# Performance work log

Measured on AMD Instinct MI355X. Metric: run time of the kernel, lower is better.

Reference implementation:

```python
import jax, jax.numpy as jnp
import numpy as np

N = 50000      # nodes
E = 800000     # edges (before self-loops)
B = 512        # graphs in batch
IN, HID, OUT, HEADS = 768, 256, 128, 4
NEG_SLOPE = 0.2
EPS = 1e-16


def glorot(key, shape):
    fan = shape[0] + shape[-1]
    return jax.random.normal(key, shape, jnp.float32) * jnp.sqrt(2.0 / fan)


def setup_inputs() -> dict:
    key = jax.random.key(0)
    ks = jax.random.split(key, 12)
    d1, d2 = HID // HEADS, OUT // HEADS
    return {
        "x": jax.random.normal(ks[0], (N, IN), jnp.float32),
        "edge_index": jax.random.randint(ks[1], (2, E), 0, N),
        "batch": jnp.sort(jax.random.randint(ks[2], (N,), 0, B)),
        # conv1: GATConv(IN, HID//HEADS, heads=HEADS)
        "W1": glorot(ks[3], (IN, HID)),
        "att_src1": glorot(ks[4], (HEADS, d1)),
        "att_dst1": glorot(ks[5], (HEADS, d1)),
        "b1": jnp.zeros((HID,), jnp.float32),
        # conv2: GATConv(HID+IN, OUT//HEADS, heads=HEADS)
        "W2": glorot(ks[6], (HID + IN, OUT)),
        "att_src2": glorot(ks[7], (HEADS, d2)),
        "att_dst2": glorot(ks[8], (HEADS, d2)),
        "b2": jnp.zeros((OUT,), jnp.float32),
    }


def gat_conv(x, src, dst, W, att_src, att_dst, bias):
    # PyG GATConv (concat heads): h = x @ W, e_ij = LeakyReLU(a_s.h_j + a_d.h_i),
    # alpha = softmax over incoming edges of each destination node.
    n = x.shape[0]
    heads, d = att_src.shape
    h = (x @ W).reshape(n, heads, d)                          # [N,H,D]
    a_s = jnp.einsum('nhd,hd->nh', h, att_src)                # [N,H]
    a_d = jnp.einsum('nhd,hd->nh', h, att_dst)
    e = jax.nn.leaky_relu(a_s[src] + a_d[dst], NEG_SLOPE)     # [Etot,H]
    e_max = jax.ops.segment_max(e, dst, num_segments=n)
    e = jnp.exp(e - e_max[dst])
    denom = jax.ops.segment_sum(e, dst, num_segments=n)
    alpha = e / (denom[dst] + EPS)                            # [Etot,H]
    msg = h[src] * alpha[:, :, None]                          # [Etot,H,D]
    out = jax.ops.segment_sum(msg, dst, num_segments=n)       # [N,H,D]
    return out.reshape(n, heads * d) + bias


def reference(x, edge_index, batch, W1, att_src1, att_dst1, b1,
              W2, att_src2, att_dst2, b2):
    # BUrumorGAT swaps edge direction: row<->col
    src = edge_index[1]
    dst = edge_index[0]
    # PyG GATConv adds self-loops by default
    loops = jnp.arange(N)
    src = jnp.concatenate([src, loops])
    dst = jnp.concatenate([dst, loops])

    x1 = x  # original features
    h1 = gat_conv(x, src, dst, W1, att_src1, att_dst1, b1)    # [N,HID]
    x2 = h1

    # root of each graph = first node (in order) with that batch id
    roots = jax.ops.segment_min(jnp.arange(N), batch, num_segments=B)  # [B]
    re1 = x1[roots[batch]]                                    # [N,IN]
    xc = jax.nn.relu(jnp.concatenate([h1, re1], axis=1))      # [N,HID+IN]
    # F.dropout with training=False is identity (eval mode)

    h2 = jax.nn.relu(gat_conv(xc, src, dst, W2, att_src2, att_dst2, b2))  # [N,OUT]
    re2 = x2[roots[batch]]                                    # [N,HID]
    feat = jnp.concatenate([h2, re2], axis=1)                 # [N,OUT+HID]

    counts = jax.ops.segment_sum(jnp.ones((N,), jnp.float32), batch, num_segments=B)
    pooled = jax.ops.segment_sum(feat, batch, num_segments=B)
    return pooled / jnp.clip(counts, 1.0)[:, None]            # [B,OUT+HID]
```

## Files before the change

kernel.cpp:

```cpp
#include <hip/hip_runtime.h>

#define NN 50000
#define NBGRAPH 512
#define DIN 768
#define DHID 256
#define DOUT 128

typedef unsigned short ushort_t;
typedef __attribute__((ext_vector_type(8))) short bf16x8;
typedef __attribute__((ext_vector_type(4))) float f32x4;
typedef _Float16 f16_t;
typedef __attribute__((ext_vector_type(8))) _Float16 f16x8;

__device__ __forceinline__ float lrelu(float v) { return v > 0.f ? v : 0.2f * v; }

__device__ __forceinline__ ushort_t f2bf(float f) {
  unsigned int u = __builtin_bit_cast(unsigned int, f);
  u += 0x7fffu + ((u >> 16) & 1u);
  return (ushort_t)(u >> 16);
}
__device__ __forceinline__ float h2f_u(ushort_t u) { return (float)__builtin_bit_cast(f16_t, u); }
__device__ __forceinline__ ushort_t f2h_u(float f) { return __builtin_bit_cast(ushort_t, (f16_t)f); }

__device__ __forceinline__ float sel_h(int h, float q0, float q1, float q2, float q3) {
  float lo = (h & 1) ? q1 : q0;
  float hi = (h & 1) ? q3 : q2;
  return (h & 2) ? hi : lo;
}

__global__ void k_zero2(int* __restrict__ a, int* __restrict__ b, int n) {
  int i = blockIdx.x * blockDim.x + threadIdx.x;
  if (i < n) { a[i] = 0; b[i] = 0; }
}

__global__ void k_hist(const int* __restrict__ ei, int* __restrict__ deg, int E, int Etot) {
  int e = blockIdx.x * blockDim.x + threadIdx.x;
  if (e >= Etot) return;
  int dst = (e < E) ? ei[e] : (e - E);
  atomicAdd(&deg[dst], 1);
}

__global__ __launch_bounds__(1024) void k_scan1(const int* __restrict__ deg, int* __restrict__ off,
                                                int* __restrict__ bsum, int n) {
  __shared__ int wsum[16];
  int tid = threadIdx.x, lane = tid & 63, w = tid >> 6;
  int i = blockIdx.x * 1024 + tid;
  int v = (i < n) ? deg[i] : 0;
  int x = v;
#pragma unroll
  for (int d = 1; d < 64; d <<= 1) { int t = __shfl_up(x, d); if (lane >= d) x += t; }
  if (lane == 63) wsum[w] = x;
  __syncthreads();
  if (tid < 16) {
    int y = wsum[tid];
#pragma unroll
    for (int d = 1; d < 16; d <<= 1) { int t = __shfl_up(y, d); if (tid >= d) y += t; }
    wsum[tid] = y;
  }
  __syncthreads();
  int base = (w > 0) ? wsum[w - 1] : 0;
  if (i < n) off[i] = base + x - v;
  if (tid == 1023) bsum[blockIdx.x] = wsum[15];
}

__global__ void k_scan2(int* __restrict__ bsum, int* __restrict__ off, int nb, int n) {
  int lane = threadIdx.x;
  int v = (lane < nb) ? bsum[lane] : 0;
  int x = v;
#pragma unroll
  for (int d = 1; d < 64; d <<= 1) { int t = __shfl_up(x, d); if (lane >= d) x += t; }
  if (lane < nb) bsum[lane] = x - v;
  if (lane == 63) off[n] = x;
}

__global__ void k_scan3(int* __restrict__ off, const int* __restrict__ bsum, int n) {
  int i = blockIdx.x * blockDim.x + threadIdx.x;
  if (i < n) off[i] += bsum[i >> 10];
}

__global__ void k_scatter(const int* __restrict__ ei, const int* __restrict__ off,
                          int* __restrict__ cur, int* __restrict__ csr, int E, int Etot) {
  int e = blockIdx.x * blockDim.x + threadIdx.x;
  if (e >= Etot) return;
  int dst, src;
  if (e < E) { dst = ei[e]; src = ei[E + e]; }
  else       { dst = src = e - E; }
  int p = atomicAdd(&cur[dst], 1);
  csr[off[dst] + p] = src;
}

__global__ void k_segstart(const int* __restrict__ batch, int* __restrict__ segstart, int n, int b_cnt) {
  int b = blockIdx.x * blockDim.x + threadIdx.x;
  if (b > b_cnt) return;
  int lo = 0, hi = n;
  while (lo < hi) { int mid = (lo + hi) >> 1; if (batch[mid] < b) lo = mid + 1; else hi = mid; }
  segstart[b] = lo;
}

__global__ void k_rootn(const int* __restrict__ batch, const int* __restrict__ segstart,
                        int* __restrict__ rootn, int n) {
  int i = blockIdx.x * blockDim.x + threadIdx.x;
  if (i < n) rootn[i] = segstart[batch[i]];
}

__global__ void k_prepW(const float* __restrict__ W, ushort_t* __restrict__ Wt, int K, int N) {
  int id = blockIdx.x * blockDim.x + threadIdx.x;
  if (id >= K * N) return;
  int n = id / K, k = id - n * K;
  Wt[(size_t)n * K + k] = f2bf(W[(size_t)k * N + n]);
}

#define LDT 40
__global__ __launch_bounds__(256) void k_gemm1m(const float* __restrict__ A,
                                                const ushort_t* __restrict__ Bt,
                                                ushort_t* __restrict__ C) {
  const int K = DIN, NC = DHID;
  __shared__ __align__(16) ushort_t As[128 * LDT];
  __shared__ __align__(16) ushort_t Bs[128 * LDT];
  const int tid = threadIdx.x;
  const int bm = blockIdx.x * 128;
  const int bn = blockIdx.y * 128;
  const int row = tid >> 1, half = tid & 1;
  const int arow = bm + row;
  const int wid = tid >> 6, lane = tid & 63;
  const int wr = (wid >> 1) * 64, wc = (wid & 1) * 64;
  const int fr = lane & 15, fg = lane >> 4;
  f32x4 acc[4][4] = {};

  for (int k0 = 0; k0 < K; k0 += 32) {
    {
      const int p = row * LDT + half * 16;
      if (arow < NN) {
        const float4* src = (const float4*)&A[(size_t)arow * K + k0 + half * 16];
#pragma unroll
        for (int i = 0; i < 4; ++i) {
          float4 v = src[i];
          ushort4 w;
          w.x = f2bf(v.x); w.y = f2bf(v.y); w.z = f2bf(v.z); w.w = f2bf(v.w);
          *(ushort4*)&As[p + i * 4] = w;
        }
      } else {
        ushort4 z = {0, 0, 0, 0};
#pragma unroll
        for (int i = 0; i < 4; ++i) *(ushort4*)&As[p + i * 4] = z;
      }
    }
#pragma unroll
    for (int i = 0; i < 2; ++i) {
      int c2 = tid + i * 256;
      int br = c2 >> 2, bq = c2 & 3;
      uint4 v = *(const uint4*)&Bt[(size_t)(bn + br) * K + k0 + bq * 8];
      *(uint4*)&Bs[br * LDT + bq * 8] = v;
    }
    __syncthreads();
    bf16x8 af[4], bfr[4];
#pragma unroll
    for (int m = 0; m < 4; ++m) af[m] = *(const bf16x8*)&As[(wr + m * 16 + fr) * LDT + fg * 8];
#pragma unroll
    for (int n = 0; n < 4; ++n) bfr[n] = *(const bf16x8*)&Bs[(wc + n * 16 + fr) * LDT + fg * 8];
#pragma unroll
    for (int m = 0; m < 4; ++m)
#pragma unroll
      for (int n = 0; n < 4; ++n)
        acc[m][n] = __builtin_amdgcn_mfma_f32_16x16x32_bf16(af[m], bfr[n], acc[m][n], 0, 0, 0);
    __syncthreads();
  }
#pragma unroll
  for (int m = 0; m < 4; ++m)
#pragma unroll
    for (int n = 0; n < 4; ++n)
#pragma unroll
      for (int j = 0; j < 4; ++j) {
        int r = bm + wr + m * 16 + fg * 4 + j;
        if (r < NN) C[(size_t)r * NC + bn + wc + n * 16 + fr] = f2h_u(acc[m][n][j]);
      }
}

__global__ __launch_bounds__(256) void k_gemm2m(const float* __restrict__ OUT1,
                                                const float* __restrict__ X,
                                                const int* __restrict__ rootn,
                                                const ushort_t* __restrict__ Bt,
                                                ushort_t* __restrict__ C) {
  const int K = DHID + DIN, NC = DOUT;
  __shared__ __align__(16) ushort_t As[128 * LDT];
  __shared__ __align__(16) ushort_t Bs[128 * LDT];
  const int tid = threadIdx.x;
  const int bm = blockIdx.x * 128;
  const int row = tid >> 1, half = tid & 1;
  const int arow = bm + row;
  const int rn = (arow < NN) ? rootn[arow] : 0;
  const int wid = tid >> 6, lane = tid & 63;
  const int wr = (wid >> 1) * 64, wc = (wid & 1) * 64;
  const int fr = lane & 15, fg = lane >> 4;
  f32x4 acc[4][4] = {};

  for (int k0 = 0; k0 < K; k0 += 32) {
    {
      const int p = row * LDT + half * 16;
      const int kk = k0 + half * 16;
      if (arow < NN) {
        const float4* src = (kk < DHID)
            ? (const float4*)&OUT1[(size_t)arow * DHID + kk]
            : (const float4*)&X[(size_t)rn * DIN + (kk - DHID)];
#pragma unroll
        for (int i = 0; i < 4; ++i) {
          float4 v = src[i];
          ushort4 w;
          w.x = f2bf(fmaxf(v.x, 0.f)); w.y = f2bf(fmaxf(v.y, 0.f));
          w.z = f2bf(fmaxf(v.z, 0.f)); w.w = f2bf(fmaxf(v.w, 0.f));
          *(ushort4*)&As[p + i * 4] = w;
        }
      } else {
        ushort4 z = {0, 0, 0, 0};
#pragma unroll
        for (int i = 0; i < 4; ++i) *(ushort4*)&As[p + i * 4] = z;
      }
    }
#pragma unroll
    for (int i = 0; i < 2; ++i) {
      int c2 = tid + i * 256;
      int br = c2 >> 2, bq = c2 & 3;
      uint4 v = *(const uint4*)&Bt[(size_t)br * K + k0 + bq * 8];
      *(uint4*)&Bs[br * LDT + bq * 8] = v;
    }
    __syncthreads();
    bf16x8 af[4], bfr[4];
#pragma unroll
    for (int m = 0; m < 4; ++m) af[m] = *(const bf16x8*)&As[(wr + m * 16 + fr) * LDT + fg * 8];
#pragma unroll
    for (int n = 0; n < 4; ++n) bfr[n] = *(const bf16x8*)&Bs[(wc + n * 16 + fr) * LDT + fg * 8];
#pragma unroll
    for (int m = 0; m < 4; ++m)
#pragma unroll
      for (int n = 0; n < 4; ++n)
        acc[m][n] = __builtin_amdgcn_mfma_f32_16x16x32_bf16(af[m], bfr[n], acc[m][n], 0, 0, 0);
    __syncthreads();
  }
#pragma unroll
  for (int m = 0; m < 4; ++m)
#pragma unroll
    for (int n = 0; n < 4; ++n)
#pragma unroll
      for (int j = 0; j < 4; ++j) {
        int r = bm + wr + m * 16 + fg * 4 + j;
        if (r < NN) C[(size_t)r * NC + wc + n * 16 + fr] = f2h_u(acc[m][n][j]);
      }
}

__global__ __launch_bounds__(256) void k_scores1(const ushort_t* __restrict__ Hh,
                                                 const float* __restrict__ att_s,
                                                 const float* __restrict__ att_d,
                                                 float4* __restrict__ as_out,
                                                 float4* __restrict__ ad_out) {
  int lane = threadIdx.x & 63;
  int n = blockIdx.x * 4 + (threadIdx.x >> 6);
  if (n >= NN) return;
  ushort4 hv = *(const ushort4*)&Hh[(size_t)n * DHID + lane * 4];
  float h0 = h2f_u(hv.x), h1 = h2f_u(hv.y), h2 = h2f_u(hv.z), h3 = h2f_u(hv.w);
  float4 sa = *(const float4*)&att_s[lane * 4];
  float4 da = *(const float4*)&att_d[lane * 4];
  float ps = h0 * sa.x + h1 * sa.y + h2 * sa.z + h3 * sa.w;
  float pd = h0 * da.x + h1 * da.y + h2 * da.z + h3 * da.w;
#pragma unroll
  for (int m = 1; m < 16; m <<= 1) { ps += __shfl_xor(ps, m); pd += __shfl_xor(pd, m); }
  float4 rs, rd;
  rs.x = __shfl(ps, 0);  rd.x = __shfl(pd, 0);
  rs.y = __shfl(ps, 16); rd.y = __shfl(pd, 16);
  rs.z = __shfl(ps, 32); rd.z = __shfl(pd, 32);
  rs.w = __shfl(ps, 48); rd.w = __shfl(pd, 48);
  if (lane == 0) { as_out[n] = rs; ad_out[n] = rd; }
}

__global__ __launch_bounds__(256) void k_scores2(const ushort_t* __restrict__ Hh,
                                                 const float* __restrict__ att_s,
                                                 const float* __restrict__ att_d,
                                                 float4* __restrict__ as_out,
                                                 float4* __restrict__ ad_out) {
  int lane = threadIdx.x & 63;
  int n = blockIdx.x * 4 + (threadIdx.x >> 6);
  if (n >= NN) return;
  ushort2 hv = *(const ushort2*)&Hh[(size_t)n * DOUT + lane * 2];
  float h0 = h2f_u(hv.x), h1 = h2f_u(hv.y);
  float2 sa = *(const float2*)&att_s[lane * 2];
  float2 da = *(const float2*)&att_d[lane * 2];
  float ps = h0 * sa.x + h1 * sa.y;
  float pd = h0 * da.x + h1 * da.y;
#pragma unroll
  for (int m = 1; m < 16; m <<= 1) { ps += __shfl_xor(ps, m); pd += __shfl_xor(pd, m); }
  float4 rs, rd;
  rs.x = __shfl(ps, 0);  rd.x = __shfl(pd, 0);
  rs.y = __shfl(ps, 16); rd.y = __shfl(pd, 16);
  rs.z = __shfl(ps, 32); rd.z = __shfl(pd, 32);
  rs.w = __shfl(ps, 48); rd.w = __shfl(pd, 48);
  if (lane == 0) { as_out[n] = rs; ad_out[n] = rd; }
}

__global__ __launch_bounds__(256) void k_agg1(const int* __restrict__ off, const int* __restrict__ csr,
                                              const float4* __restrict__ as_v, const float4* __restrict__ ad_v,
                                              const ushort_t* __restrict__ Hh, const float* __restrict__ bias,
                                              float* __restrict__ OUT) {
  __shared__ int s_tab[16][65];
  __shared__ __align__(16) float al_tab[16][260];
  const int tid = threadIdx.x;
  const int nd = tid >> 4;
  const int g = tid & 15;
  const int hd = g >> 2;
  const int n = blockIdx.x * 16 + nd;
  if (n >= NN) return;
  const int beg = off[n];
  const int nt = off[n + 1] - beg;
  const float4 adv = ad_v[n];

  float acc[16] = {};
  float rdh;

  if (nt <= 64) {
    float mx0 = -INFINITY, mx1 = -INFINITY, mx2 = -INFINITY, mx3 = -INFINITY;
    for (int le = g; le < nt; le += 16) {
      int s = csr[beg + le];
      float4 a = as_v[s];
      s_tab[nd][le] = s;
      *(float4*)&al_tab[nd][le << 2] = a;
      mx0 = fmaxf(mx0, a.x); mx1 = fmaxf(mx1, a.y);
      mx2 = fmaxf(mx2, a.z); mx3 = fmaxf(mx3, a.w);
    }
#pragma unroll
    for (int m = 1; m < 16; m <<= 1) {
      mx0 = fmaxf(mx0, __shfl_xor(mx0, m)); mx1 = fmaxf(mx1, __shfl_xor(mx1, m));
      mx2 = fmaxf(mx2, __shfl_xor(mx2, m)); mx3 = fmaxf(mx3, __shfl_xor(mx3, m));
    }
    float em0 = lrelu(mx0 + adv.x), em1 = lrelu(mx1 + adv.y);
    float em2 = lrelu(mx2 + adv.z), em3 = lrelu(mx3 + adv.w);
    float s0 = 0.f, s1 = 0.f, s2 = 0.f, s3 = 0.f;
    for (int le = g; le < nt; le += 16) {
      float4 a = *(const float4*)&al_tab[nd][le << 2];
      float p0 = __expf(lrelu(a.x + adv.x) - em0);
      float p1 = __expf(lrelu(a.y + adv.y) - em1);
      float p2 = __expf(lrelu(a.z + adv.z) - em2);
      float p3 = __expf(lrelu(a.w + adv.w) - em3);
      *(float4*)&al_tab[nd][le << 2] = make_float4(p0, p1, p2, p3);
      s0 += p0; s1 += p1; s2 += p2; s3 += p3;
    }
#pragma unroll
    for (int m = 1; m < 16; m <<= 1) {
      s0 += __shfl_xor(s0, m); s1 += __shfl_xor(s1, m);
      s2 += __shfl_xor(s2, m); s3 += __shfl_xor(s3, m);
    }
    float r0 = 1.f / (s0 + 1e-16f), r1 = 1.f / (s1 + 1e-16f);
    float r2 = 1.f / (s2 + 1e-16f), r3 = 1.f / (s3 + 1e-16f);
    rdh = sel_h(hd, r0, r1, r2, r3);

    int sP = s_tab[nd][0];
    float pP = al_tab[nd][hd];
    f16x8 v0 = *(const f16x8*)&Hh[(size_t)sP * DHID + g * 16];
    f16x8 v1 = *(const f16x8*)&Hh[(size_t)sP * DHID + g * 16 + 8];
    for (int e = 0; e < nt; ++e) {
      int en = (e + 1 < nt) ? e + 1 : e;
      int sN = s_tab[nd][en];
      float pN = al_tab[nd][(en << 2) | hd];
      f16x8 n0 = *(const f16x8*)&Hh[(size_t)sN * DHID + g * 16];
      f16x8 n1 = *(const f16x8*)&Hh[(size_t)sN * DHID + g * 16 + 8];
      float al = pP * rdh;
#pragma unroll
      for (int q = 0; q < 8; ++q) acc[q] += al * (float)v0[q];
#pragma unroll
      for (int q = 0; q < 8; ++q) acc[8 + q] += al * (float)v1[q];
      pP = pN; v0 = n0; v1 = n1;
    }
  } else {
    float mx0 = -INFINITY, mx1 = -INFINITY, mx2 = -INFINITY, mx3 = -INFINITY;
    for (int le = g; le < nt; le += 16) {
      float4 a = as_v[csr[beg + le]];
      mx0 = fmaxf(mx0, a.x); mx1 = fmaxf(mx1, a.y);
      mx2 = fmaxf(mx2, a.z); mx3 = fmaxf(mx3, a.w);
    }
#pragma unroll
    for (int m = 1; m < 16; m <<= 1) {
      mx0 = fmaxf(mx0, __shfl_xor(mx0, m)); mx1 = fmaxf(mx1, __shfl_xor(mx1, m));
      mx2 = fmaxf(mx2, __shfl_xor(mx2, m)); mx3 = fmaxf(mx3, __shfl_xor(mx3, m));
    }
    float em0 = lrelu(mx0 + adv.x), em1 = lrelu(mx1 + adv.y);
    float em2 = lrelu(mx2 + adv.z), em3 = lrelu(mx3 + adv.w);
    float s0 = 0.f, s1 = 0.f, s2 = 0.f, s3 = 0.f;
    for (int le = g; le < nt; le += 16) {
      float4 a = as_v[csr[beg + le]];
      s0 += __expf(lrelu(a.x + adv.x) - em0);
      s1 += __expf(lrelu(a.y + adv.y) - em1);
      s2 += __expf(lrelu(a.z + adv.z) - em2);
      s3 += __expf(lrelu(a.w + adv.w) - em3);
    }
#pragma unroll
    for (int m = 1; m < 16; m <<= 1) {
      s0 += __shfl_xor(s0, m); s1 += __shfl_xor(s1, m);
      s2 += __shfl_xor(s2, m); s3 += __shfl_xor(s3, m);
    }
    rdh = sel_h(hd, 1.f / (s0 + 1e-16f), 1.f / (s1 + 1e-16f),
                    1.f / (s2 + 1e-16f), 1.f / (s3 + 1e-16f));
    float adh = sel_h(hd, adv.x, adv.y, adv.z, adv.w);
    float emh = sel_h(hd, em0, em1, em2, em3);
    for (int e = 0; e < nt; ++e) {
      int s = csr[beg + e];
      float4 a = as_v[s];
      float ah = sel_h(hd, a.x, a.y, a.z, a.w);
      float al = __expf(lrelu(ah + adh) - emh) * rdh;
      f16x8 v0 = *(const f16x8*)&Hh[(size_t)s * DHID + g * 16];
      f16x8 v1 = *(const f16x8*)&Hh[(size_t)s * DHID + g * 16 + 8];
#pragma unroll
      for (int q = 0; q < 8; ++q) acc[q] += al * (float)v0[q];
#pragma unroll
      for (int q = 0; q < 8; ++q) acc[8 + q] += al * (float)v1[q];
    }
  }

  const float* bv = &bias[g * 16];
  float* ob = &OUT[(size_t)n * DHID + g * 16];
#pragma unroll
  for (int k = 0; k < 4; ++k) {
    float4 b4 = *(const float4*)&bv[k * 4];
    *(float4*)&ob[k * 4] = make_float4(acc[k * 4] + b4.x, acc[k * 4 + 1] + b4.y,
                                       acc[k * 4 + 2] + b4.z, acc[k * 4 + 3] + b4.w);
  }
}

__global__ __launch_bounds__(256) void k_agg2(const int* __restrict__ off, const int* __restrict__ csr,
                                              const float4* __restrict__ as_v, const float4* __restrict__ ad_v,
                                              const ushort_t* __restrict__ Hh, const float* __restrict__ bias,
                                              float* __restrict__ OUT) {
  __shared__ int s_tab[16][65];
  __shared__ __align__(16) float al_tab[16][260];
  const int tid = threadIdx.x;
  const int nd = tid >> 4;
  const int g = tid & 15;
  const int hd = g >> 2;
// ... 77 lines not shown
      s3 += __expf(lrelu(a.w + adv.w) - em3);
    }
#pragma unroll
    for (int m = 1; m < 16; m <<= 1) {
      s0 += __shfl_xor(s0, m); s1 += __shfl_xor(s1, m);
      s2 += __shfl_xor(s2, m); s3 += __shfl_xor(s3, m);
    }
    rdh = sel_h(hd, 1.f / (s0 + 1e-16f), 1.f / (s1 + 1e-16f),
                    1.f / (s2 + 1e-16f), 1.f / (s3 + 1e-16f));
    float adh = sel_h(hd, adv.x, adv.y, adv.z, adv.w);
    float emh = sel_h(hd, em0, em1, em2, em3);
    for (int e = 0; e < nt; ++e) {
      int s = csr[beg + e];
      float4 a = as_v[s];
      float ah = sel_h(hd, a.x, a.y, a.z, a.w);
      float al = __expf(lrelu(ah + adh) - emh) * rdh;
      f16x8 v0 = *(const f16x8*)&Hh[(size_t)s * DOUT + g * 8];
#pragma unroll
      for (int q = 0; q < 8; ++q) acc[q] += al * (float)v0[q];
    }
  }

  const float* bv = &bias[g * 8];
  float* ob = &OUT[(size_t)n * DOUT + g * 8];
#pragma unroll
  for (int k = 0; k < 2; ++k) {
    float4 b4 = *(const float4*)&bv[k * 4];
    *(float4*)&ob[k * 4] = make_float4(acc[k * 4] + b4.x, acc[k * 4 + 1] + b4.y,
                                       acc[k * 4 + 2] + b4.z, acc[k * 4 + 3] + b4.w);
  }
}

__global__ __launch_bounds__(256) void k_pool(const int* __restrict__ segstart,
                                              const float* __restrict__ OUT2,
                                              const float* __restrict__ OUT1,
                                              float* __restrict__ out) {
  int b = blockIdx.x;
  int t = threadIdx.x;
  int s = segstart[b], e = segstart[b + 1];
  float* ob = out + (size_t)b * 384;
  if (s >= e) {
    for (int i = t; i < 384; i += 256) ob[i] = 0.f;
    return;
  }
  if (t < 128) {
    float s0 = 0.f, s1 = 0.f;
    int n = s;
    for (; n + 1 < e; n += 2) {
      float v0 = OUT2[(size_t)n * DOUT + t];
      float v1 = OUT2[(size_t)(n + 1) * DOUT + t];
      s0 += fmaxf(v0, 0.f); s1 += fmaxf(v1, 0.f);
    }
    if (n < e) s0 += fmaxf(OUT2[(size_t)n * DOUT + t], 0.f);
    ob[t] = (s0 + s1) / (float)(e - s);
  } else {
    int k = t - 128;
    ob[128 + k] = OUT1[(size_t)s * DHID + k];
    ob[256 + k] = OUT1[(size_t)s * DHID + 128 + k];
  }
}

extern "C" void kernel_launch(void* const* d_in, const int* in_sizes, int n_in,
                              void* d_out, int out_size, void* d_ws, size_t ws_size,
                              hipStream_t stream) {
  const float* x    = (const float*)d_in[0];
  const int*   ei   = (const int*)d_in[1];
  const int*   batch = (const int*)d_in[2];
  const float* W1   = (const float*)d_in[3];
  const float* as1w = (const float*)d_in[4];
  const float* ad1w = (const float*)d_in[5];
  const float* b1   = (const float*)d_in[6];
  const float* W2   = (const float*)d_in[7];
  const float* as2w = (const float*)d_in[8];
  const float* ad2w = (const float*)d_in[9];
  const float* b2   = (const float*)d_in[10];
  float* out = (float*)d_out;
  char* ws = (char*)d_ws;

  const int E = in_sizes[1] / 2;
  const int Etot = E + NN;

  ushort_t* H1h = (ushort_t*)(ws + 0);
  ushort_t* H2h = (ushort_t*)(ws + 0);
  ushort_t* Wt2b = (ushort_t*)(ws + 13000000);
  float*  OUT2 = (float*)(ws + 25600000);
  float*  OUT1 = (float*)(ws + 51200000);
  float4* as1  = (float4*)(ws + 102400000);
  float4* ad1  = (float4*)(ws + 103200000);
  float4* as2  = (float4*)(ws + 104000000);
  float4* ad2  = (float4*)(ws + 104800000);
  int* deg     = (int*)(ws + 105600000);
  int* cur     = (int*)(ws + 105800000);
  int* off     = (int*)(ws + 106000000);
  int* csr     = (int*)(ws + 106200016);
  int* segstart = (int*)(ws + 109600016);
  int* rootn   = (int*)(ws + 109602080);
  int* bsum    = (int*)(ws + 109802080);
  ushort_t* Wt1b = (ushort_t*)(ws + 105600000);

  const int TB = 256;
  const int NB_SCAN = (NN + 1023) / 1024;

  k_zero2<<<(NN + TB - 1) / TB, TB, 0, stream>>>(deg, cur, NN);
  k_hist<<<(Etot + TB - 1) / TB, TB, 0, stream>>>(ei, deg, E, Etot);
  k_scan1<<<NB_SCAN, 1024, 0, stream>>>(deg, off, bsum, NN);
  k_scan2<<<1, 64, 0, stream>>>(bsum, off, NB_SCAN, NN);
  k_scan3<<<NB_SCAN, 1024, 0, stream>>>(off, bsum, NN);
  k_scatter<<<(Etot + TB - 1) / TB, TB, 0, stream>>>(ei, off, cur, csr, E, Etot);
  k_segstart<<<(NBGRAPH + 1 + TB - 1) / TB, TB, 0, stream>>>(batch, segstart, NN, NBGRAPH);
  k_rootn<<<(NN + TB - 1) / TB, TB, 0, stream>>>(batch, segstart, rootn, NN);

  k_prepW<<<(DIN * DHID + TB - 1) / TB, TB, 0, stream>>>(W1, Wt1b, DIN, DHID);
  dim3 g1((NN + 127) / 128, DHID / 128);
  k_gemm1m<<<g1, TB, 0, stream>>>(x, Wt1b, H1h);
  k_scores1<<<(NN + 3) / 4, TB, 0, stream>>>(H1h, as1w, ad1w, as1, ad1);
  k_agg1<<<(NN + 15) / 16, TB, 0, stream>>>(off, csr, as1, ad1, H1h, b1, OUT1);

  k_prepW<<<((DHID + DIN) * DOUT + TB - 1) / TB, TB, 0, stream>>>(W2, Wt2b, DHID + DIN, DOUT);
  dim3 g2((NN + 127) / 128, 1);
  k_gemm2m<<<g2, TB, 0, stream>>>(OUT1, x, rootn, Wt2b, H2h);
  k_scores2<<<(NN + 3) / 4, TB, 0, stream>>>(H2h, as2w, ad2w, as2, ad2);
  k_agg2<<<(NN + 15) / 16, TB, 0, stream>>>(off, csr, as2, ad2, H2h, b2, OUT2);

  k_pool<<<NBGRAPH, TB, 0, stream>>>(segstart, OUT2, OUT1, out);
}
```

Measured before the change: 372.0 us.

## Rewrite both GEMMs to load MFMA fragments directly from global memory in fp16

Both dense GEMM kernels drop LDS staging and __syncthreads. Each wave now loads its A and B fragments straight from global memory into registers, converts A with packed fp16 conversion, and issues fp16 MFMAs. The tile shrinks from 128 to 64 rows per block so more blocks are launched, and the weights are stored as fp16 instead of bf16. This removes LDS traffic and barriers at the cost of less data reuse across waves and extra redundant global loads. In gemm2 the root-feature gather is split into a separate K loop.

```diff
diff --git a/kernel.cpp b/kernel.cpp
--- a/kernel.cpp
+++ b/kernel.cpp
@@ -7,18 +7,13 @@
 #define DOUT 128
 
 typedef unsigned short ushort_t;
-typedef __attribute__((ext_vector_type(8))) short bf16x8;
 typedef __attribute__((ext_vector_type(4))) float f32x4;
 typedef _Float16 f16_t;
+typedef __attribute__((ext_vector_type(2))) _Float16 f16x2;
 typedef __attribute__((ext_vector_type(8))) _Float16 f16x8;
 
 __device__ __forceinline__ float lrelu(float v) { return v > 0.f ? v : 0.2f * v; }
 
-__device__ __forceinline__ ushort_t f2bf(float f) {
-  unsigned int u = __builtin_bit_cast(unsigned int, f);
-  u += 0x7fffu + ((u >> 16) & 1u);
-  return (ushort_t)(u >> 16);
-}
 __device__ __forceinline__ float h2f_u(ushort_t u) { return (float)__builtin_bit_cast(f16_t, u); }
 __device__ __forceinline__ ushort_t f2h_u(float f) { return __builtin_bit_cast(ushort_t, (f16_t)f); }
 
@@ -26,6 +21,20 @@
   float lo = (h & 1) ? q1 : q0;
   float hi = (h & 1) ? q3 : q2;
   return (h & 2) ? hi : lo;
+}
+
+__device__ __forceinline__ f16x8 cvt8(float4 u, float4 v) {
+  unsigned int a = __builtin_bit_cast(unsigned int, __builtin_amdgcn_cvt_pkrtz(u.x, u.y));
+  unsigned int b = __builtin_bit_cast(unsigned int, __builtin_amdgcn_cvt_pkrtz(u.z, u.w));
+  unsigned int c = __builtin_bit_cast(unsigned int, __builtin_amdgcn_cvt_pkrtz(v.x, v.y));
+  unsigned int d = __builtin_bit_cast(unsigned int, __builtin_amdgcn_cvt_pkrtz(v.z, v.w));
+  uint4 q = {a, b, c, d};
+  return __builtin_bit_cast(f16x8, q);
+}
+__device__ __forceinline__ f16x8 cvt8_relu(float4 u, float4 v) {
+  u.x = fmaxf(u.x, 0.f); u.y = fmaxf(u.y, 0.f); u.z = fmaxf(u.z, 0.f); u.w = fmaxf(u.w, 0.f);
+  v.x = fmaxf(v.x, 0.f); v.y = fmaxf(v.y, 0.f); v.z = fmaxf(v.z, 0.f); v.w = fmaxf(v.w, 0.f);
+  return cvt8(u, v);
 }
 
 __global__ void k_zero2(int* __restrict__ a, int* __restrict__ b, int n) {
@@ -107,66 +116,54 @@
   int id = blockIdx.x * blockDim.x + threadIdx.x;
   if (id >= K * N) return;
   int n = id / K, k = id - n * K;
-  Wt[(size_t)n * K + k] = f2bf(W[(size_t)k * N + n]);
-}
-
-#define LDT 40
+  Wt[(size_t)n * K + k] = f2h_u(W[(size_t)k * N + n]);
+}
+
 __global__ __launch_bounds__(256) void k_gemm1m(const float* __restrict__ A,
                                                 const ushort_t* __restrict__ Bt,
                                                 ushort_t* __restrict__ C) {
   const int K = DIN, NC = DHID;
-  __shared__ __align__(16) ushort_t As[128 * LDT];
-  __shared__ __align__(16) ushort_t Bs[128 * LDT];
   const int tid = threadIdx.x;
-  const int bm = blockIdx.x * 128;
+  const int bm = blockIdx.x * 64;
   const int bn = blockIdx.y * 128;
-  const int row = tid >> 1, half = tid & 1;
-  const int arow = bm + row;
   const int wid = tid >> 6, lane = tid & 63;
-  const int wr = (wid >> 1) * 64, wc = (wid & 1) * 64;
+  const int wr = (wid >> 1) * 32, wc = (wid & 1) * 64;
   const int fr = lane & 15, fg = lane >> 4;
-  f32x4 acc[4][4] = {};
-
+  const int row0 = bm + wr + fr;
+  const int row1 = bm + wr + 16 + fr;
+  const int r0c = row0 < NN ? row0 : NN - 1;
+  const int r1c = row1 < NN ? row1 : NN - 1;
+  const float* a0 = &A[(size_t)r0c * K + fg * 8];
+  const float* a1 = &A[(size_t)r1c * K + fg * 8];
+  const ushort_t* b0 = &Bt[(size_t)(bn + wc + fr) * K + fg * 8];
+  const ushort_t* b1 = &Bt[(size_t)(bn + wc + 16 + fr) * K + fg * 8];
+  const ushort_t* b2 = &Bt[(size_t)(bn + wc + 32 + fr) * K + fg * 8];
+  const ushort_t* b3 = &Bt[(size_t)(bn + wc + 48 + fr) * K + fg * 8];
+  f32x4 acc[2][4] = {};
+
+#pragma unroll 4
   for (int k0 = 0; k0 < K; k0 += 32) {
-    {
-      const int p = row * LDT + half * 16;
-      if (arow < NN) {
-        const float4* src = (const float4*)&A[(size_t)arow * K + k0 + half * 16];
-#pragma unroll
-        for (int i = 0; i < 4; ++i) {
-          float4 v = src[i];
-          ushort4 w;
-          w.x = f2bf(v.x); w.y = f2bf(v.y); w.z = f2bf(v.z); w.w = f2bf(v.w);
-          *(ushort4*)&As[p + i * 4] = w;
-        }
-      } else {
-        ushort4 z = {0, 0, 0, 0};
-#pragma unroll
-        for (int i = 0; i < 4; ++i) *(ushort4*)&As[p + i * 4] = z;
-      }
-    }
-#pragma unroll
-    for (int i = 0; i < 2; ++i) {
-      int c2 = tid + i * 256;
-      int br = c2 >> 2, bq = c2 & 3;
-      uint4 v = *(const uint4*)&Bt[(size_t)(bn + br) * K + k0 + bq * 8];
-      *(uint4*)&Bs[br * LDT + bq * 8] = v;
-    }
-    __syncthreads();
-    bf16x8 af[4], bfr[4];
-#pragma unroll
-    for (int m = 0; m < 4; ++m) af[m] = *(const bf16x8*)&As[(wr + m * 16 + fr) * LDT + fg * 8];
-#pragma unroll
-    for (int n = 0; n < 4; ++n) bfr[n] = *(const bf16x8*)&Bs[(wc + n * 16 + fr) * LDT + fg * 8];
-#pragma unroll
-    for (int m = 0; m < 4; ++m)
-#pragma unroll
-      for (int n = 0; n < 4; ++n)
-        acc[m][n] = __builtin_amdgcn_mfma_f32_16x16x32_bf16(af[m], bfr[n], acc[m][n], 0, 0, 0);
-    __syncthreads();
-  }
-#pragma unroll
-  for (int m = 0; m < 4; ++m)
+    float4 u0 = *(const float4*)(a0 + k0);
+    float4 v0 = *(const float4*)(a0 + k0 + 4);
+    float4 u1 = *(const float4*)(a1 + k0);
+    float4 v1 = *(const float4*)(a1 + k0 + 4);
+    f16x8 bf0 = *(const f16x8*)(b0 + k0);
+    f16x8 bf1 = *(const f16x8*)(b1 + k0);
+    f16x8 bf2 = *(const f16x8*)(b2 + k0);
+    f16x8 bf3 = *(const f16x8*)(b3 + k0);
+    f16x8 af0 = cvt8(u0, v0);
+    f16x8 af1 = cvt8(u1, v1);
+    acc[0][0] = __builtin_amdgcn_mfma_f32_16x16x32_f16(af0, bf0, acc[0][0], 0, 0, 0);
+    acc[0][1] = __builtin_amdgcn_mfma_f32_16x16x32_f16(af0, bf1, acc[0][1], 0, 0, 0);
+    acc[0][2] = __builtin_amdgcn_mfma_f32_16x16x32_f16(af0, bf2, acc[0][2], 0, 0, 0);
+    acc[0][3] = __builtin_amdgcn_mfma_f32_16x16x32_f16(af0, bf3, acc[0][3], 0, 0, 0);
+    acc[1][0] = __builtin_amdgcn_mfma_f32_16x16x32_f16(af1, bf0, acc[1][0], 0, 0, 0);
+    acc[1][1] = __builtin_amdgcn_mfma_f32_16x16x32_f16(af1, bf1, acc[1][1], 0, 0, 0);
+    acc[1][2] = __builtin_amdgcn_mfma_f32_16x16x32_f16(af1, bf2, acc[1][2], 0, 0, 0);
+    acc[1][3] = __builtin_amdgcn_mfma_f32_16x16x32_f16(af1, bf3, acc[1][3], 0, 0, 0);
+  }
+#pragma unroll
+  for (int m = 0; m < 2; ++m)
 #pragma unroll
     for (int n = 0; n < 4; ++n)
 #pragma unroll
@@ -182,62 +179,71 @@
                                                 const ushort_t* __restrict__ Bt,
                                                 ushort_t* __restrict__ C) {
   const int K = DHID + DIN, NC = DOUT;
-  __shared__ __align__(16) ushort_t As[128 * LDT];
-  __shared__ __align__(16) ushort_t Bs[128 * LDT];
   const int tid = threadIdx.x;
-  const int bm = blockIdx.x * 128;
-  const int row = tid >> 1, half = tid & 1;
-  const int arow = bm + row;
-  const int rn = (arow < NN) ? rootn[arow] : 0;
+  const int bm = blockIdx.x * 64;
   const int wid = tid >> 6, lane = tid & 63;
-  const int wr = (wid >> 1) * 64, wc = (wid & 1) * 64;
+  const int wr = (wid >> 1) * 32, wc = (wid & 1) * 64;
   const int fr = lane & 15, fg = lane >> 4;
-  f32x4 acc[4][4] = {};
-
-  for (int k0 = 0; k0 < K; k0 += 32) {
-    {
-      const int p = row * LDT + half * 16;
-      const int kk = k0 + half * 16;
-      if (arow < NN) {
-        const float4* src = (kk < DHID)
-            ? (const float4*)&OUT1[(size_t)arow * DHID + kk]
-            : (const float4*)&X[(size_t)rn * DIN + (kk - DHID)];
-#pragma unroll
-        for (int i = 0; i < 4; ++i) {
-          float4 v = src[i];
-          ushort4 w;
-          w.x = f2bf(fmaxf(v.x, 0.f)); w.y = f2bf(fmaxf(v.y, 0.f));
-          w.z = f2bf(fmaxf(v.z, 0.f)); w.w = f2bf(fmaxf(v.w, 0.f));
-          *(ushort4*)&As[p + i * 4] = w;
-        }
-      } else {
-        ushort4 z = {0, 0, 0, 0};
-#pragma unroll
-        for (int i = 0; i < 4; ++i) *(ushort4*)&As[p + i * 4] = z;
-      }
-    }
-#pragma unroll
-    for (int i = 0; i < 2; ++i) {
-      int c2 = tid + i * 256;
-      int br = c2 >> 2, bq = c2 & 3;
-      uint4 v = *(const uint4*)&Bt[(size_t)br * K + k0 + bq * 8];
-      *(uint4*)&Bs[br * LDT + bq * 8] = v;
-    }
-    __syncthreads();
-    bf16x8 af[4], bfr[4];
-#pragma unroll
-    for (int m = 0; m < 4; ++m) af[m] = *(const bf16x8*)&As[(wr + m * 16 + fr) * LDT + fg * 8];
-#pragma unroll
-    for (int n = 0; n < 4; ++n) bfr[n] = *(const bf16x8*)&Bs[(wc + n * 16 + fr) * LDT + fg * 8];
-#pragma unroll
-    for (int m = 0; m < 4; ++m)
-#pragma unroll
-      for (int n = 0; n < 4; ++n)
-        acc[m][n] = __builtin_amdgcn_mfma_f32_16x16x32_bf16(af[m], bfr[n], acc[m][n], 0, 0, 0);
-    __syncthreads();
-  }
-#pragma unroll
-  for (int m = 0; m < 4; ++m)
+  const int row0 = bm + wr + fr;
+  const int row1 = bm + wr + 16 + fr;
+  const int r0c = row0 < NN ? row0 : NN - 1;
+  const int r1c = row1 < NN ? row1 : NN - 1;
+  const int rn0 = rootn[r0c];
+  const int rn1 = rootn[r1c];
+  const float* o0 = &OUT1[(size_t)r0c * DHID + fg * 8];
+  const float* o1 = &OUT1[(size_t)r1c * DHID + fg * 8];
+  const float* x0 = &X[(size_t)rn0 * DIN + fg * 8];
+  const float* x1 = &X[(size_t)rn1 * DIN + fg * 8];
+  const ushort_t* b0 = &Bt[(size_t)(wc + fr) * K + fg * 8];
+  const ushort_t* b1 = &Bt[(size_t)(wc + 16 + fr) * K + fg * 8];
+  const ushort_t* b2 = &Bt[(size_t)(wc + 32 + fr) * K + fg * 8];
+  const ushort_t* b3 = &Bt[(size_t)(wc + 48 + fr) * K + fg * 8];
+  f32x4 acc[2][4] = {};
+
+#pragma unroll 4
+  for (int k0 = 0; k0 < DHID; k0 += 32) {
+    float4 u0 = *(const float4*)(o0 + k0);
+    float4 v0 = *(const float4*)(o0 + k0 + 4);
+    float4 u1 = *(const float4*)(o1 + k0);
+    float4 v1 = *(const float4*)(o1 + k0 + 4);
+    f16x8 bf0 = *(const f16x8*)(b0 + k0);
+    f16x8 bf1 = *(const f16x8*)(b1 + k0);
+    f16x8 bf2 = *(const f16x8*)(b2 + k0);
+    f16x8 bf3 = *(const f16x8*)(b3 + k0);
+    f16x8 af0 = cvt8_relu(u0, v0);
+    f16x8 af1 = cvt8_relu(u1, v1);
+    acc[0][0] = __builtin_amdgcn_mfma_f32_16x16x32_f16(af0, bf0, acc[0][0], 0, 0, 0);
+    acc[0][1] = __builtin_amdgcn_mfma_f32_16x16x32_f16(af0, bf1, acc[0][1], 0, 0, 0);
+    acc[0][2] = __builtin_amdgcn_mfma_f32_16x16x32_f16(af0, bf2, acc[0][2], 0, 0, 0);
+    acc[0][3] = __builtin_amdgcn_mfma_f32_16x16x32_f16(af0, bf3, acc[0][3], 0, 0, 0);
+    acc[1][0] = __builtin_amdgcn_mfma_f32_16x16x32_f16(af1, bf0, acc[1][0], 0, 0, 0);
+    acc[1][1] = __builtin_amdgcn_mfma_f32_16x16x32_f16(af1, bf1, acc[1][1], 0, 0, 0);
+    acc[1][2] = __builtin_amdgcn_mfma_f32_16x16x32_f16(af1, bf2, acc[1][2], 0, 0, 0);
+    acc[1][3] = __builtin_amdgcn_mfma_f32_16x16x32_f16(af1, bf3, acc[1][3], 0, 0, 0);
+  }
+#pragma unroll 4
+  for (int k0 = 0; k0 < DIN; k0 += 32) {
+    float4 u0 = *(const float4*)(x0 + k0);
+    float4 v0 = *(const float4*)(x0 + k0 + 4);
+    float4 u1 = *(const float4*)(x1 + k0);
+    float4 v1 = *(const float4*)(x1 + k0 + 4);
+    f16x8 bf0 = *(const f16x8*)(b0 + DHID + k0);
+    f16x8 bf1 = *(const f16x8*)(b1 + DHID + k0);
+    f16x8 bf2 = *(const f16x8*)(b2 + DHID + k0);
+    f16x8 bf3 = *(const f16x8*)(b3 + DHID + k0);
+    f16x8 af0 = cvt8_relu(u0, v0);
+    f16x8 af1 = cvt8_relu(u1, v1);
+    acc[0][0] = __builtin_amdgcn_mfma_f32_16x16x32_f16(af0, bf0, acc[0][0], 0, 0, 0);
+    acc[0][1] = __builtin_amdgcn_mfma_f32_16x16x32_f16(af0, bf1, acc[0][1], 0, 0, 0);
+    acc[0][2] = __builtin_amdgcn_mfma_f32_16x16x32_f16(af0, bf2, acc[0][2], 0, 0, 0);
+    acc[0][3] = __builtin_amdgcn_mfma_f32_16x16x32_f16(af0, bf3, acc[0][3], 0, 0, 0);
+    acc[1][0] = __builtin_amdgcn_mfma_f32_16x16x32_f16(af1, bf0, acc[1][0], 0, 0, 0);
+    acc[1][1] = __builtin_amdgcn_mfma_f32_16x16x32_f16(af1, bf1, acc[1][1], 0, 0, 0);
+    acc[1][2] = __builtin_amdgcn_mfma_f32_16x16x32_f16(af1, bf2, acc[1][2], 0, 0, 0);
+    acc[1][3] = __builtin_amdgcn_mfma_f32_16x16x32_f16(af1, bf3, acc[1][3], 0, 0, 0);
+  }
+#pragma unroll
+  for (int m = 0; m < 2; ++m)
 #pragma unroll
     for (int n = 0; n < 4; ++n)
 #pragma unroll
@@ -346,9 +352,8 @@
       s0 += __shfl_xor(s0, m); s1 += __shfl_xor(s1, m);
       s2 += __shfl_xor(s2, m); s3 += __shfl_xor(s3, m);
     }
-    float r0 = 1.f / (s0 + 1e-16f), r1 = 1.f / (s1 + 1e-16f);
-    float r2 = 1.f / (s2 + 1e-16f), r3 = 1.f / (s3 + 1e-16f);
-    rdh = sel_h(hd, r0, r1, r2, r3);
+    rdh = sel_h(hd, 1.f / (s0 + 1e-16f), 1.f / (s1 + 1e-16f),
+                    1.f / (s2 + 1e-16f), 1.f / (s3 + 1e-16f));
 
     int sP = s_tab[nd][0];
     float pP = al_tab[nd][hd];
@@ -592,7 +597,7 @@
 
   ushort_t* H1h = (ushort_t*)(ws + 0);
   ushort_t* H2h = (ushort_t*)(ws + 0);
-  ushort_t* Wt2b = (ushort_t*)(ws + 13000000);
+  ushort_t* Wt2h = (ushort_t*)(ws + 13000000);
   float*  OUT2 = (float*)(ws + 25600000);
   float*  OUT1 = (float*)(ws + 51200000);
   float4* as1  = (float4*)(ws + 102400000);
@@ -606,7 +611,7 @@
   int* segstart = (int*)(ws + 109600016);
   int* rootn   = (int*)(ws + 109602080);
   int* bsum    = (int*)(ws + 109802080);
-  ushort_t* Wt1b = (ushort_t*)(ws + 105600000);
+  ushort_t* Wt1h = (ushort_t*)(ws + 105600000);
 
   const int TB = 256;
   const int NB_SCAN = (NN + 1023) / 1024;
@@ -620,15 +625,15 @@
   k_segstart<<<(NBGRAPH + 1 + TB - 1) / TB, TB, 0, stream>>>(batch, segstart, NN, NBGRAPH);
   k_rootn<<<(NN + TB - 1) / TB, TB, 0, stream>>>(batch, segstart, rootn, NN);
 
-  k_prepW<<<(DIN * DHID + TB - 1) / TB, TB, 0, stream>>>(W1, Wt1b, DIN, DHID);
-  dim3 g1((NN + 127) / 128, DHID / 128);
-  k_gemm1m<<<g1, TB, 0, stream>>>(x, Wt1b, H1h);
+  k_prepW<<<(DIN * DHID + TB - 1) / TB, TB, 0, stream>>>(W1, Wt1h, DIN, DHID);
+  dim3 g1((NN + 63) / 64, DHID / 128);
+  k_gemm1m<<<g1, TB, 0, stream>>>(x, Wt1h, H1h);
   k_scores1<<<(NN + 3) / 4, TB, 0, stream>>>(H1h, as1w, ad1w, as1, ad1);
   k_agg1<<<(NN + 15) / 16, TB, 0, stream>>>(off, csr, as1, ad1, H1h, b1, OUT1);
 
-  k_prepW<<<((DHID + DIN) * DOUT + TB - 1) / TB, TB, 0, stream>>>(W2, Wt2b, DHID + DIN, DOUT);
-  dim3 g2((NN + 127) / 128, 1);
-  k_gemm2m<<<g2, TB, 0, stream>>>(OUT1, x, rootn, Wt2b, H2h);
+  k_prepW<<<((DHID + DIN) * DOUT + TB - 1) / TB, TB, 0, stream>>>(W2, Wt2h, DHID + DIN, DOUT);
+  dim3 g2((NN + 63) / 64, 1);
+  k_gemm2m<<<g2, TB, 0, stream>>>(OUT1, x, rootn, Wt2h, H2h);
   k_scores2<<<(NN + 3) / 4, TB, 0, stream>>>(H2h, as2w, ad2w, as2, ad2);
   k_agg2<<<(NN + 15) / 16, TB, 0, stream>>>(off, csr, as2, ad2, H2h, b2, OUT2);
 
```

Measured after the change: 492.2 us. 32.3% more time.

## Load GEMM tiles via direct global-to-LDS, switch to fp16 MFMA with swizzled LDS

Applied to the files above, without the earlier changes.

Both GEMM kernels now stage raw fp32 A tiles and fp16 B tiles straight into LDS with global_load_lds, using an XOR-swizzled layout in place of padding. Conversion from fp32 to fp16 (plus ReLU for the second GEMM) moves to after the LDS read, just before the MFMA, which now uses the f16 variant instead of bf16. The goal is to drop the register round-trip and the per-element conversion on the global-load path, and to avoid bank conflicts. In exchange the A tile in LDS doubles in size, every wave repeats the conversion work, and fp16 trades range for mantissa compared with bf16.

```diff
diff --git a/kernel.cpp b/kernel.cpp
--- a/kernel.cpp
+++ b/kernel.cpp
@@ -7,18 +7,12 @@
 #define DOUT 128
 
 typedef unsigned short ushort_t;
-typedef __attribute__((ext_vector_type(8))) short bf16x8;
 typedef __attribute__((ext_vector_type(4))) float f32x4;
 typedef _Float16 f16_t;
 typedef __attribute__((ext_vector_type(8))) _Float16 f16x8;
 
 __device__ __forceinline__ float lrelu(float v) { return v > 0.f ? v : 0.2f * v; }
 
-__device__ __forceinline__ ushort_t f2bf(float f) {
-  unsigned int u = __builtin_bit_cast(unsigned int, f);
-  u += 0x7fffu + ((u >> 16) & 1u);
-  return (ushort_t)(u >> 16);
-}
 __device__ __forceinline__ float h2f_u(ushort_t u) { return (float)__builtin_bit_cast(f16_t, u); }
 __device__ __forceinline__ ushort_t f2h_u(float f) { return __builtin_bit_cast(ushort_t, (f16_t)f); }
 
@@ -26,6 +20,26 @@
   float lo = (h & 1) ? q1 : q0;
   float hi = (h & 1) ? q3 : q2;
   return (h & 2) ? hi : lo;
+}
+
+__device__ __forceinline__ f16x8 cvt8(float4 u, float4 v) {
+  unsigned int a = __builtin_bit_cast(unsigned int, __builtin_amdgcn_cvt_pkrtz(u.x, u.y));
+  unsigned int b = __builtin_bit_cast(unsigned int, __builtin_amdgcn_cvt_pkrtz(u.z, u.w));
+  unsigned int c = __builtin_bit_cast(unsigned int, __builtin_amdgcn_cvt_pkrtz(v.x, v.y));
+  unsigned int d = __builtin_bit_cast(unsigned int, __builtin_amdgcn_cvt_pkrtz(v.z, v.w));
+  uint4 q = {a, b, c, d};
+  return __builtin_bit_cast(f16x8, q);
+}
+__device__ __forceinline__ f16x8 cvt8_relu(float4 u, float4 v) {
+  u.x = fmaxf(u.x, 0.f); u.y = fmaxf(u.y, 0.f); u.z = fmaxf(u.z, 0.f); u.w = fmaxf(u.w, 0.f);
+  v.x = fmaxf(v.x, 0.f); v.y = fmaxf(v.y, 0.f); v.z = fmaxf(v.z, 0.f); v.w = fmaxf(v.w, 0.f);
+  return cvt8(u, v);
+}
+
+__device__ __forceinline__ void gl_lds16(const void* g, void* l) {
+  __builtin_amdgcn_global_load_lds(
+      (const __attribute__((address_space(1))) unsigned int*)g,
+      (__attribute__((address_space(3))) unsigned int*)l, 16, 0, 0);
 }
 
 __global__ void k_zero2(int* __restrict__ a, int* __restrict__ b, int n) {
@@ -107,62 +121,70 @@
   int id = blockIdx.x * blockDim.x + threadIdx.x;
   if (id >= K * N) return;
   int n = id / K, k = id - n * K;
-  Wt[(size_t)n * K + k] = f2bf(W[(size_t)k * N + n]);
-}
-
-#define LDT 40
+  Wt[(size_t)n * K + k] = f2h_u(W[(size_t)k * N + n]);
+}
+
 __global__ __launch_bounds__(256) void k_gemm1m(const float* __restrict__ A,
                                                 const ushort_t* __restrict__ Bt,
                                                 ushort_t* __restrict__ C) {
   const int K = DIN, NC = DHID;
-  __shared__ __align__(16) ushort_t As[128 * LDT];
-  __shared__ __align__(16) ushort_t Bs[128 * LDT];
+  __shared__ __align__(16) float As[128 * 32];
+  __shared__ __align__(16) ushort_t Bs[128 * 32];
   const int tid = threadIdx.x;
   const int bm = blockIdx.x * 128;
   const int bn = blockIdx.y * 128;
-  const int row = tid >> 1, half = tid & 1;
-  const int arow = bm + row;
   const int wid = tid >> 6, lane = tid & 63;
   const int wr = (wid >> 1) * 64, wc = (wid & 1) * 64;
   const int fr = lane & 15, fg = lane >> 4;
   f32x4 acc[4][4] = {};
 
+  const float* asrc[4];
+  float* adst[4];
+#pragma unroll
+  for (int j = 0; j < 4; ++j) {
+    int c = j * 256 + tid;
+    int row = c >> 3, ci = c & 7;
+    int gc = ci ^ (row & 7);
+    int gr = bm + row; if (gr >= NN) gr = NN - 1;
+    asrc[j] = &A[(size_t)gr * K + gc * 4];
+    adst[j] = &As[row * 32 + ci * 4];
+  }
+  const ushort_t* bsrc[2];
+  ushort_t* bdst[2];
+#pragma unroll
+  for (int j = 0; j < 2; ++j) {
+    int c = j * 256 + tid;
+    int col = c >> 2, ci = c & 3;
+    int gc = ci ^ (col & 3);
+    bsrc[j] = &Bt[(size_t)(bn + col) * K + gc * 8];
+    bdst[j] = &Bs[col * 32 + ci * 8];
+  }
+
   for (int k0 = 0; k0 < K; k0 += 32) {
-    {
-      const int p = row * LDT + half * 16;
-      if (arow < NN) {
-        const float4* src = (const float4*)&A[(size_t)arow * K + k0 + half * 16];
-#pragma unroll
-        for (int i = 0; i < 4; ++i) {
-          float4 v = src[i];
-          ushort4 w;
-          w.x = f2bf(v.x); w.y = f2bf(v.y); w.z = f2bf(v.z); w.w = f2bf(v.w);
-          *(ushort4*)&As[p + i * 4] = w;
-        }
-      } else {
-        ushort4 z = {0, 0, 0, 0};
-#pragma unroll
-        for (int i = 0; i < 4; ++i) *(ushort4*)&As[p + i * 4] = z;
-      }
-    }
-#pragma unroll
-    for (int i = 0; i < 2; ++i) {
-      int c2 = tid + i * 256;
-      int br = c2 >> 2, bq = c2 & 3;
-      uint4 v = *(const uint4*)&Bt[(size_t)(bn + br) * K + k0 + bq * 8];
-      *(uint4*)&Bs[br * LDT + bq * 8] = v;
-    }
+#pragma unroll
+    for (int j = 0; j < 4; ++j) gl_lds16(asrc[j] + k0, adst[j]);
+#pragma unroll
+    for (int j = 0; j < 2; ++j) gl_lds16(bsrc[j] + k0, bdst[j]);
     __syncthreads();
-    bf16x8 af[4], bfr[4];
-#pragma unroll
-    for (int m = 0; m < 4; ++m) af[m] = *(const bf16x8*)&As[(wr + m * 16 + fr) * LDT + fg * 8];
-#pragma unroll
-    for (int n = 0; n < 4; ++n) bfr[n] = *(const bf16x8*)&Bs[(wc + n * 16 + fr) * LDT + fg * 8];
+    f16x8 af[4], bfr[4];
+#pragma unroll
+    for (int m = 0; m < 4; ++m) {
+      int r = wr + m * 16 + fr;
+      int c0 = (2 * fg) ^ (r & 7), c1 = (2 * fg + 1) ^ (r & 7);
+      float4 u = *(const float4*)&As[r * 32 + c0 * 4];
+      float4 v = *(const float4*)&As[r * 32 + c1 * 4];
+      af[m] = cvt8(u, v);
+    }
+#pragma unroll
+    for (int n = 0; n < 4; ++n) {
+      int c = wc + n * 16 + fr;
+      bfr[n] = *(const f16x8*)&Bs[c * 32 + (fg ^ (c & 3)) * 8];
+    }
 #pragma unroll
     for (int m = 0; m < 4; ++m)
 #pragma unroll
       for (int n = 0; n < 4; ++n)
-        acc[m][n] = __builtin_amdgcn_mfma_f32_16x16x32_bf16(af[m], bfr[n], acc[m][n], 0, 0, 0);
+        acc[m][n] = __builtin_amdgcn_mfma_f32_16x16x32_f16(af[m], bfr[n], acc[m][n], 0, 0, 0);
     __syncthreads();
   }
 #pragma unroll
@@ -182,58 +204,67 @@
                                                 const ushort_t* __restrict__ Bt,
                                                 ushort_t* __restrict__ C) {
   const int K = DHID + DIN, NC = DOUT;
-  __shared__ __align__(16) ushort_t As[128 * LDT];
-  __shared__ __align__(16) ushort_t Bs[128 * LDT];
+  __shared__ __align__(16) float As[128 * 32];
+  __shared__ __align__(16) ushort_t Bs[128 * 32];
   const int tid = threadIdx.x;
   const int bm = blockIdx.x * 128;
-  const int row = tid >> 1, half = tid & 1;
-  const int arow = bm + row;
-  const int rn = (arow < NN) ? rootn[arow] : 0;
   const int wid = tid >> 6, lane = tid & 63;
   const int wr = (wid >> 1) * 64, wc = (wid & 1) * 64;
   const int fr = lane & 15, fg = lane >> 4;
   f32x4 acc[4][4] = {};
 
+  const float* o1src[4];
+  const float* xsrc[4];
+  float* adst[4];
+#pragma unroll
+  for (int j = 0; j < 4; ++j) {
+    int c = j * 256 + tid;
+    int row = c >> 3, ci = c & 7;
+    int gc = ci ^ (row & 7);
+    int gr = bm + row; if (gr >= NN) gr = NN - 1;
+    int rn = rootn[gr];
+    o1src[j] = &OUT1[(size_t)gr * DHID + gc * 4];
+    xsrc[j] = &X[(size_t)rn * DIN + gc * 4];
+    adst[j] = &As[row * 32 + ci * 4];
+  }
+  const ushort_t* bsrc[2];
+  ushort_t* bdst[2];
+#pragma unroll
+  for (int j = 0; j < 2; ++j) {
+    int c = j * 256 + tid;
+    int col = c >> 2, ci = c & 3;
+    int gc = ci ^ (col & 3);
+    bsrc[j] = &Bt[(size_t)col * K + gc * 8];
+    bdst[j] = &Bs[col * 32 + ci * 8];
+  }
+
   for (int k0 = 0; k0 < K; k0 += 32) {
-    {
-      const int p = row * LDT + half * 16;
-      const int kk = k0 + half * 16;
-      if (arow < NN) {
-        const float4* src = (kk < DHID)
-            ? (const float4*)&OUT1[(size_t)arow * DHID + kk]
-            : (const float4*)&X[(size_t)rn * DIN + (kk - DHID)];
-#pragma unroll
-        for (int i = 0; i < 4; ++i) {
-          float4 v = src[i];
-          ushort4 w;
-          w.x = f2bf(fmaxf(v.x, 0.f)); w.y = f2bf(fmaxf(v.y, 0.f));
-          w.z = f2bf(fmaxf(v.z, 0.f)); w.w = f2bf(fmaxf(v.w, 0.f));
-          *(ushort4*)&As[p + i * 4] = w;
-        }
-      } else {
-        ushort4 z = {0, 0, 0, 0};
-#pragma unroll
-        for (int i = 0; i < 4; ++i) *(ushort4*)&As[p + i * 4] = z;
-      }
-    }
-#pragma unroll
-    for (int i = 0; i < 2; ++i) {
-      int c2 = tid + i * 256;
-      int br = c2 >> 2, bq = c2 & 3;
-      uint4 v = *(const uint4*)&Bt[(size_t)br * K + k0 + bq * 8];
-      *(uint4*)&Bs[br * LDT + bq * 8] = v;
-    }
+    const bool inO1 = k0 < DHID;
+#pragma unroll
+    for (int j = 0; j < 4; ++j)
+      gl_lds16(inO1 ? (o1src[j] + k0) : (xsrc[j] + (k0 - DHID)), adst[j]);
+#pragma unroll
+    for (int j = 0; j < 2; ++j) gl_lds16(bsrc[j] + k0, bdst[j]);
     __syncthreads();
-    bf16x8 af[4], bfr[4];
-#pragma unroll
-    for (int m = 0; m < 4; ++m) af[m] = *(const bf16x8*)&As[(wr + m * 16 + fr) * LDT + fg * 8];
-#pragma unroll
-    for (int n = 0; n < 4; ++n) bfr[n] = *(const bf16x8*)&Bs[(wc + n * 16 + fr) * LDT + fg * 8];
+    f16x8 af[4], bfr[4];
+#pragma unroll
+    for (int m = 0; m < 4; ++m) {
+      int r = wr + m * 16 + fr;
+      int c0 = (2 * fg) ^ (r & 7), c1 = (2 * fg + 1) ^ (r & 7);
+      float4 u = *(const float4*)&As[r * 32 + c0 * 4];
+      float4 v = *(const float4*)&As[r * 32 + c1 * 4];
+      af[m] = cvt8_relu(u, v);
+    }
+#pragma unroll
+    for (int n = 0; n < 4; ++n) {
+      int c = wc + n * 16 + fr;
+      bfr[n] = *(const f16x8*)&Bs[c * 32 + (fg ^ (c & 3)) * 8];
+    }
 #pragma unroll
     for (int m = 0; m < 4; ++m)
 #pragma unroll
       for (int n = 0; n < 4; ++n)
-        acc[m][n] = __builtin_amdgcn_mfma_f32_16x16x32_bf16(af[m], bfr[n], acc[m][n], 0, 0, 0);
+        acc[m][n] = __builtin_amdgcn_mfma_f32_16x16x32_f16(af[m], bfr[n], acc[m][n], 0, 0, 0);
     __syncthreads();
   }
 #pragma unroll
@@ -346,9 +377,8 @@
       s0 += __shfl_xor(s0, m); s1 += __shfl_xor(s1, m);
       s2 += __shfl_xor(s2, m); s3 += __shfl_xor(s3, m);
     }
-    float r0 = 1.f / (s0 + 1e-16f), r1 = 1.f / (s1 + 1e-16f);
-    float r2 = 1.f / (s2 + 1e-16f), r3 = 1.f / (s3 + 1e-16f);
-    rdh = sel_h(hd, r0, r1, r2, r3);
+    rdh = sel_h(hd, 1.f / (s0 + 1e-16f), 1.f / (s1 + 1e-16f),
+                    1.f / (s2 + 1e-16f), 1.f / (s3 + 1e-16f));
 
     int sP = s_tab[nd][0];
     float pP = al_tab[nd][hd];
@@ -592,7 +622,7 @@
 
   ushort_t* H1h = (ushort_t*)(ws + 0);
   ushort_t* H2h = (ushort_t*)(ws + 0);
-  ushort_t* Wt2b = (ushort_t*)(ws + 13000000);
+  ushort_t* Wt2h = (ushort_t*)(ws + 13000000);
   float*  OUT2 = (float*)(ws + 25600000);
   float*  OUT1 = (float*)(ws + 51200000);
   float4* as1  = (float4*)(ws + 102400000);
@@ -606,7 +636,7 @@
   int* segstart = (int*)(ws + 109600016);
   int* rootn   = (int*)(ws + 109602080);
   int* bsum    = (int*)(ws + 109802080);
-  ushort_t* Wt1b = (ushort_t*)(ws + 105600000);
+  ushort_t* Wt1h = (ushort_t*)(ws + 105600000);
 
   const int TB = 256;
   const int NB_SCAN = (NN + 1023) / 1024;
@@ -620,15 +650,15 @@
   k_segstart<<<(NBGRAPH + 1 + TB - 1) / TB, TB, 0, stream>>>(batch, segstart, NN, NBGRAPH);
   k_rootn<<<(NN + TB - 1) / TB, TB, 0, stream>>>(batch, segstart, rootn, NN);
 
-  k_prepW<<<(DIN * DHID + TB - 1) / TB, TB, 0, stream>>>(W1, Wt1b, DIN, DHID);
+  k_prepW<<<(DIN * DHID + TB - 1) / TB, TB, 0, stream>>>(W1, Wt1h, DIN, DHID);
   dim3 g1((NN + 127) / 128, DHID / 128);
-  k_gemm1m<<<g1, TB, 0, stream>>>(x, Wt1b, H1h);
+  k_gemm1m<<<g1, TB, 0, stream>>>(x, Wt1h, H1h);
   k_scores1<<<(NN + 3) / 4, TB, 0, stream>>>(H1h, as1w, ad1w, as1, ad1);
   k_agg1<<<(NN + 15) / 16, TB, 0, stream>>>(off, csr, as1, ad1, H1h, b1, OUT1);
 
-  k_prepW<<<((DHID + DIN) * DOUT + TB - 1) / TB, TB, 0, stream>>>(W2, Wt2b, DHID + DIN, DOUT);
+  k_prepW<<<((DHID + DIN) * DOUT + TB - 1) / TB, TB, 0, stream>>>(W2, Wt2h, DHID + DIN, DOUT);
   dim3 g2((NN + 127) / 128, 1);
-  k_gemm2m<<<g2, TB, 0, stream>>>(OUT1, x, rootn, Wt2b, H2h);
+  k_gemm2m<<<g2, TB, 0, stream>>>(OUT1, x, rootn, Wt2h, H2h);
   k_scores2<<<(NN + 3) / 4, TB, 0, stream>>>(H2h, as2w, ad2w, as2, ad2);
   k_agg2<<<(NN + 15) / 16, TB, 0, stream>>>(off, csr, as2, ad2, H2h, b2, OUT2);
 
```

Result: faster. 354.2 us (-4.8%).
